# Optimization experiments

Measured on AMD Instinct MI355X. Metric: run time of the kernel, lower is better.

The kernel has to match this reference:

```python
import jax, jax.numpy as jnp
import numpy as np

B, T, D_MODEL, HEAD_DIM = 4, 4096, 2048, 128
NEG = -1e9  # matches torch's -1000000000.0 mask fill


def setup_inputs() -> dict:
    key = jax.random.key(0)
    ks = jax.random.split(key, 7)
    s = 0.02
    return {
        "x": jax.random.normal(ks[0], (B, T, D_MODEL), dtype=jnp.float32),
        "q_w": jax.random.normal(ks[1], (HEAD_DIM, D_MODEL), dtype=jnp.float32) * s,
        "q_b": jax.random.normal(ks[2], (HEAD_DIM,), dtype=jnp.float32) * s,
        "k_w": jax.random.normal(ks[3], (HEAD_DIM, D_MODEL), dtype=jnp.float32) * s,
        "k_b": jax.random.normal(ks[4], (HEAD_DIM,), dtype=jnp.float32) * s,
        "v_w": jax.random.normal(ks[5], (HEAD_DIM, D_MODEL), dtype=jnp.float32) * s,
        "v_b": jax.random.normal(ks[6], (HEAD_DIM,), dtype=jnp.float32) * s,
    }


def reference(x, q_w, q_b, k_w, k_b, v_w, v_b):
    # Linear projections: y = x @ W^T + b  -> [B, T, head_dim]
    q = jnp.einsum("btc,hc->bth", x, q_w) + q_b
    k = jnp.einsum("btc,hc->bth", x, k_w) + k_b
    v = jnp.einsum("btc,hc->bth", x, v_w) + v_b

    head_dim = q.shape[-1]
    # scores [B, T, T], scaled by 1/sqrt(head_dim)
    scores = jnp.einsum("bqh,bkh->bqk", q, k) / jnp.sqrt(jnp.float32(head_dim))
    # causal mask: additive -1e9 above the diagonal (future positions)
    t = scores.shape[-1]
    mask = jnp.triu(jnp.full((t, t), NEG, dtype=scores.dtype), k=1)
    scores = scores + mask
    probs = jax.nn.softmax(scores, axis=-1)
    # dropout p=0.0 -> identity (eval)
    y = jnp.einsum("bqk,bkh->bqh", probs, v)
    return y
```

## Files before the change

### kernel.cpp

```cpp
#include <hip/hip_runtime.h>

#define T_SEQ 4096
#define DMODEL 2048
#define HD 128

typedef float f32x4 __attribute__((ext_vector_type(4)));
typedef _Float16 f16x8 __attribute__((ext_vector_type(8)));

__device__ __forceinline__ unsigned short f2h(float f) {
  union { _Float16 h; unsigned short u; } v;
  v.h = (_Float16)f;
  return v.u;
}

__device__ __forceinline__ unsigned pk2h(float lo, float hi) {
  return (unsigned)f2h(lo) | ((unsigned)f2h(hi) << 16);
}

template <int CTRL>
__device__ __forceinline__ float dppmax(float x) {
  union { float f; int i; } a, b;
  a.f = x;
  b.i = __builtin_amdgcn_update_dpp(a.i, a.i, CTRL, 0xF, 0xF, false);
  return fmaxf(x, b.f);
}
template <int CTRL>
__device__ __forceinline__ float dppadd(float x) {
  union { float f; int i; } a, b;
  a.f = x;
  b.i = __builtin_amdgcn_update_dpp(a.i, a.i, CTRL, 0xF, 0xF, false);
  return x + b.f;
}
__device__ __forceinline__ float red16_max(float x) {
  x = dppmax<0xB1>(x); x = dppmax<0x4E>(x);
  x = dppmax<0x124>(x); x = dppmax<0x128>(x);
  return x;
}
__device__ __forceinline__ float red16_add(float x) {
  x = dppadd<0xB1>(x); x = dppadd<0x4E>(x);
  x = dppadd<0x124>(x); x = dppadd<0x128>(x);
  return x;
}

__global__ __launch_bounds__(256) void cvt_w_kernel(
    const float* __restrict__ qw, const float* __restrict__ qb,
    const float* __restrict__ kw, const float* __restrict__ kb,
    const float* __restrict__ vw, const float* __restrict__ vb,
    unsigned short* __restrict__ wb, float* __restrict__ biasc) {
  int idx = blockIdx.x * 256 + threadIdx.x;
  int e = idx * 4;
  int row = e >> 11;
  int col = e & 2047;
  const float* src = (row < 128) ? (qw + row * 2048)
                   : (row < 256) ? (kw + (row - 128) * 2048)
                                 : (vw + (row - 256) * 2048);
  float4 v = *(const float4*)(src + col);
  ushort4 o;
  o.x = f2h(v.x); o.y = f2h(v.y); o.z = f2h(v.z); o.w = f2h(v.w);
  *(ushort4*)(wb + e) = o;
  if (blockIdx.x == 0 && threadIdx.x < 384) {
    int n = threadIdx.x;
    biasc[n] = (n < 128) ? qb[n] : (n < 256) ? kb[n - 128] : vb[n - 256];
  }
}

#define SAB 40
__global__ __launch_bounds__(256, 3) void proj_kernel(
    const float* __restrict__ x, const unsigned short* __restrict__ wb,
    const float* __restrict__ biasc, unsigned short* __restrict__ qkv) {
  __shared__ unsigned short sA[64 * SAB];
  __shared__ unsigned short sB[128 * SAB];
  const int tid = threadIdx.x;
  const int lane = tid & 63;
  const int w = tid >> 6;
  const int fr = lane & 15;
  const int g = lane >> 4;
  const int m0 = blockIdx.x * 64;
  const int n0 = blockIdx.y * 128;
  const int wm = (w & 1) * 32;
  const int wn = (w >> 1) * 64;

  const int arow = tid >> 2;
  const int acolA = (tid & 3) * 8;
  const int brow = tid >> 1;
  const int bcolB = (tid & 1) * 16;
  const float* xp = x + (size_t)(m0 + arow) * DMODEL + acolA;
  const unsigned short* bp = wb + (size_t)(n0 + brow) * DMODEL + bcolB;

  f32x4 acc[2][4] = {};
  float4 ax0 = *(const float4*)(xp);
  float4 ax1 = *(const float4*)(xp + 4);
  uint4 bx0 = *(const uint4*)(bp);
  uint4 bx1 = *(const uint4*)(bp + 8);

  for (int k0 = 0; k0 < DMODEL; k0 += 32) {
    __syncthreads();
    uint4 pa;
    pa.x = pk2h(ax0.x, ax0.y); pa.y = pk2h(ax0.z, ax0.w);
    pa.z = pk2h(ax1.x, ax1.y); pa.w = pk2h(ax1.z, ax1.w);
    *(uint4*)&sA[arow * SAB + acolA] = pa;
    *(uint4*)&sB[brow * SAB + bcolB] = bx0;
    *(uint4*)&sB[brow * SAB + bcolB + 8] = bx1;
    __syncthreads();

    if (k0 + 32 < DMODEL) {
      ax0 = *(const float4*)(xp + k0 + 32);
      ax1 = *(const float4*)(xp + k0 + 36);
      bx0 = *(const uint4*)(bp + k0 + 32);
      bx1 = *(const uint4*)(bp + k0 + 40);
    }

    f16x8 af[2], bf[4];
#pragma unroll
    for (int i = 0; i < 2; ++i)
      af[i] = *(const f16x8*)&sA[(wm + 16 * i + fr) * SAB + g * 8];
#pragma unroll
    for (int jn = 0; jn < 4; ++jn)
      bf[jn] = *(const f16x8*)&sB[(wn + 16 * jn + fr) * SAB + g * 8];
#pragma unroll
    for (int i = 0; i < 2; ++i)
#pragma unroll
      for (int jn = 0; jn < 4; ++jn)
        acc[i][jn] = __builtin_amdgcn_mfma_f32_16x16x32_f16(af[i], bf[jn], acc[i][jn], 0, 0, 0);
  }

#pragma unroll
  for (int jn = 0; jn < 4; ++jn) {
    int n = n0 + wn + 16 * jn + fr;
    float bias = biasc[n];
#pragma unroll
    for (int i = 0; i < 2; ++i) {
      int mb = m0 + wm + 16 * i + g * 4;
#pragma unroll
      for (int r = 0; r < 4; ++r)
        qkv[(size_t)(mb + r) * 384 + n] = f2h(acc[i][jn][r] + bias);
    }
  }
}

#define SKS 136
#define SVS 72
#define SPS 72
__global__ __launch_bounds__(256) __attribute__((amdgpu_waves_per_eu(2, 3)))
void attn_kernel(
    const unsigned short* __restrict__ qkv, float* __restrict__ out,
    float* __restrict__ po, float* __restrict__ pml, int split) {
  __shared__ unsigned short sK[64 * SKS];
  __shared__ unsigned short sVt[128 * SVS];
  __shared__ unsigned short sP[64 * SPS];
  const int id = blockIdx.x;
  const int batch = blockIdx.y;
  int qt, c, nc;
  if (split) {
    if (id < 16)      { qt = id;                c = 0;          nc = 1; }
    else if (id < 48) { qt = 16 + ((id - 16) >> 1); c = (id - 16) & 1; nc = 2; }
    else if (id < 96) { qt = 32 + (id - 48) / 3;    c = (id - 48) % 3; nc = 3; }
    else              { qt = 48 + ((id - 96) >> 2); c = (id - 96) & 3; nc = 4; }
  } else { qt = id; c = 0; nc = 1; }
  const int qbase = qt * 64;
  const int ntl = qt + 1;
  const int t0 = (c * ntl) / nc;
  const int tend = ((c + 1) * ntl) / nc;
  const int tid = threadIdx.x;
  const int lane = tid & 63;
  const int w = tid >> 6;
  const int fr = lane & 15;
  const int g = lane >> 4;
  const int va = tid >> 4;
  const int vu = tid & 15;
  const int vblk = ((va ^ (vu & 14)) << 2);
  const unsigned short* qkvb = qkv + (size_t)batch * T_SEQ * 384;

  f16x8 qf[4];
  {
    const unsigned short* qp = qkvb + (size_t)(qbase + 16 * w + fr) * 384 + g * 8;
#pragma unroll
    for (int s = 0; s < 4; ++s) qf[s] = *(const f16x8*)(qp + 32 * s);
  }
  f32x4 o[8] = {};
  float m_r[4], l_r[4];
#pragma unroll
  for (int r = 0; r < 4; ++r) { m_r[r] = -1e30f; l_r[r] = 0.f; }
  const float scale = 0.08838834764831845f;

  uint4 pk[4], pvv[4];
#pragma unroll
  for (int it = 0; it < 4; ++it) {
    int idx = it * 256 + tid;
    pk[it] = *(const uint4*)(qkvb + (size_t)(t0 * 64 + (idx >> 4)) * 384 + 128 + (idx & 15) * 8);
  }
#pragma unroll
  for (int i = 0; i < 4; ++i)
    pvv[i] = *(const uint4*)(qkvb + (size_t)(t0 * 64 + va + 16 * i) * 384 + 256 + vu * 8);

  for (int t = t0; t < tend; ++t) {
    const int kbase = t * 64;
    __syncthreads();
#pragma unroll
    for (int it = 0; it < 4; ++it) {
      int idx = it * 256 + tid;
      *(uint4*)&sK[(idx >> 4) * SKS + (idx & 15) * 8] = pk[it];
    }
    {
      const unsigned* w0 = (const unsigned*)&pvv[0];
      const unsigned* w1 = (const unsigned*)&pvv[1];
      const unsigned* w2 = (const unsigned*)&pvv[2];
      const unsigned* w3 = (const unsigned*)&pvv[3];
#pragma unroll
      for (int j2 = 0; j2 < 4; ++j2) {
        uint2 se, so;
        se.x = __builtin_amdgcn_perm(w1[j2], w0[j2], 0x05040100);
        se.y = __builtin_amdgcn_perm(w3[j2], w2[j2], 0x05040100);
        so.x = __builtin_amdgcn_perm(w1[j2], w0[j2], 0x07060302);
        so.y = __builtin_amdgcn_perm(w3[j2], w2[j2], 0x07060302);
        *(uint2*)&sVt[(8 * vu + 2 * j2) * SVS + vblk] = se;
        *(uint2*)&sVt[(8 * vu + 2 * j2 + 1) * SVS + vblk] = so;
      }
    }
    __syncthreads();

    if (t + 1 < tend) {
#pragma unroll
      for (int it = 0; it < 4; ++it) {
        int idx = it * 256 + tid;
        pk[it] = *(const uint4*)(qkvb + (size_t)((t + 1) * 64 + (idx >> 4)) * 384 + 128 + (idx & 15) * 8);
      }
#pragma unroll
      for (int i = 0; i < 4; ++i)
        pvv[i] = *(const uint4*)(qkvb + (size_t)((t + 1) * 64 + va + 16 * i) * 384 + 256 + vu * 8);
    }

    f32x4 sacc[4] = {};
#pragma unroll
    for (int ks = 0; ks < 4; ++ks)
#pragma unroll
      for (int tn = 0; tn < 4; ++tn) {
        f16x8 kf = *(const f16x8*)&sK[(16 * tn + fr) * SKS + 32 * ks + g * 8];
        sacc[tn] = __builtin_amdgcn_mfma_f32_16x16x32_f16(qf[ks], kf, sacc[tn], 0, 0, 0);
      }

    const bool diag = (t == qt);
#pragma unroll
    for (int r = 0; r < 4; ++r) {
      int grow = qbase + 16 * w + g * 4 + r;
      float s0 = sacc[0][r] * scale;
      float s1 = sacc[1][r] * scale;
      float s2 = sacc[2][r] * scale;
      float s3 = sacc[3][r] * scale;
      if (diag) {
        int kd = grow - kbase - fr;
        if (0 > kd)  s0 = -1e30f;
        if (16 > kd) s1 = -1e30f;
        if (32 > kd) s2 = -1e30f;
        if (48 > kd) s3 = -1e30f;
      }
      float mx = fmaxf(fmaxf(s0, s1), fmaxf(s2, s3));
      mx = red16_max(mx);
      float mnew = fmaxf(m_r[r], mx);
      float alpha = __expf(m_r[r] - mnew);
      m_r[r] = mnew;
      float p0 = __expf(s0 - mnew);
      float p1 = __expf(s1 - mnew);
      float p2 = __expf(s2 - mnew);
      float p3 = __expf(s3 - mnew);
      float rs = (p0 + p1) + (p2 + p3);
      rs = red16_add(rs);
      l_r[r] = l_r[r] * alpha + rs;
#pragma unroll
      for (int nt = 0; nt < 8; ++nt) o[nt][r] *= alpha;
      uint2 pw;
      pw.x = pk2h(p0, p1);
      pw.y = pk2h(p2, p3);
      *(uint2*)&sP[(16 * w + 4 * g + r) * SPS + 4 * fr] = pw;
    }

#pragma unroll
    for (int ks = 0; ks < 2; ++ks) {
      f16x8 pa = *(const f16x8*)&sP[(16 * w + fr) * SPS + 32 * ks + 8 * g];
#pragma unroll
      for (int nt = 0; nt < 8; ++nt) {
        int d = 16 * nt + fr;
        int blk = ((8 * ks + 2 * g) ^ ((d >> 3) & 14)) << 2;
        f16x8 vf = *(const f16x8*)&sVt[d * SVS + blk];
        o[nt] = __builtin_amdgcn_mfma_f32_16x16x32_f16(pa, vf, o[nt], 0, 0, 0);
      }
    }
  }

  if (nc == 1) {
#pragma unroll
    for (int r = 0; r < 4; ++r) {
      float inv = 1.0f / l_r[r];
      int grow = qbase + 16 * w + g * 4 + r;
      float* op = out + ((size_t)batch * T_SEQ + grow) * HD;
#pragma unroll
      for (int nt = 0; nt < 8; ++nt)
        op[16 * nt + fr] = o[nt][r] * inv;
    }
  } else {
    size_t slot = ((size_t)batch * 160 + id) * 64;
#pragma unroll
    for (int r = 0; r < 4; ++r) {
      int lrow = 16 * w + g * 4 + r;
      float* op = po + (slot + lrow) * 128;
#pragma unroll
      for (int nt = 0; nt < 8; ++nt)
        op[16 * nt + fr] = o[nt][r];
      if (fr == 0) {
        pml[(slot + lrow) * 2] = m_r[r];
        pml[(slot + lrow) * 2 + 1] = l_r[r];
      }
    }
  }
}

__global__ __launch_bounds__(256) void combine_kernel(
    const float* __restrict__ po, const float* __restrict__ pml,
    float* __restrict__ out) {
  int gr = blockIdx.x * 2 + (threadIdx.x >> 7);
  int d = threadIdx.x & 127;
  int batch = gr / 3072;
  int ridx = gr - batch * 3072;
  int qt = 16 + (ridx >> 6);
  int rr = ridx & 63;
  int nc = 1 + (qt >> 4);
  int sb = (qt < 32) ? 16 + (qt - 16) * 2
         : (qt < 48) ? 48 + (qt - 32) * 3
                     : 96 + (qt - 48) * 4;
  size_t base = ((size_t)batch * 160 + sb) * 64 + rr;
  float mi[4], li[4];
  float M = -1e30f;
#pragma unroll
  for (int i = 0; i < 4; ++i) {
    if (i < nc) {
      mi[i] = pml[(base + (size_t)i * 64) * 2];
      li[i] = pml[(base + (size_t)i * 64) * 2 + 1];
      M = fmaxf(M, mi[i]);
    }
  }
  float L = 0.f, acc = 0.f;
#pragma unroll
  for (int i = 0; i < 4; ++i) {
    if (i < nc) {
      float sc = __expf(mi[i] - M);
      L += li[i] * sc;
      acc += po[(base + (size_t)i * 64) * 128 + d] * sc;
    }
  }
  out[((size_t)batch * T_SEQ + qt * 64 + rr) * HD + d] = acc / L;
}

extern "C" void kernel_launch(void* const* d_in, const int* in_sizes, int n_in,
                              void* d_out, int out_size, void* d_ws, size_t ws_size,
                              hipStream_t stream) {
  const float* x  = (const float*)d_in[0];
  const float* qw = (const float*)d_in[1];
  const float* qb = (const float*)d_in[2];
  const float* kw = (const float*)d_in[3];
  const float* kb = (const float*)d_in[4];
  const float* vw = (const float*)d_in[5];
  const float* vb = (const float*)d_in[6];
  float* out = (float*)d_out;

  unsigned short* qkv = (unsigned short*)d_ws;
  unsigned short* wb  = qkv + (size_t)16384 * 384;
  float* biasc = (float*)(wb + (size_t)384 * 2048);
  float* po  = (float*)((char*)d_ws + 14157312);
  float* pml = po + (size_t)640 * 64 * 128;
  size_t need = 14157312 + (size_t)640 * 64 * 128 * 4 + (size_t)640 * 64 * 2 * 4;
  int split = (ws_size >= need) ? 1 : 0;

  cvt_w_kernel<<<768, 256, 0, stream>>>(qw, qb, kw, kb, vw, vb, wb, biasc);
  proj_kernel<<<dim3(256, 3), 256, 0, stream>>>(x, wb, biasc, qkv);
  attn_kernel<<<dim3(split ? 160 : 64, 4), 256, 0, stream>>>(qkv, out, po, pml, split);
  if (split)
    combine_kernel<<<6144, 256, 0, stream>>>(po, pml, out);
}
```

Before: 142.0 us.

## Double attention query tile to 128 rows with 512-thread blocks sharing K/V tiles

```diff
diff --git a/kernel.cpp b/kernel.cpp
--- a/kernel.cpp
+++ b/kernel.cpp
@@ -141,24 +141,24 @@
 #define SKS 136
 #define SVS 72
 #define SPS 72
-__global__ __launch_bounds__(256) __attribute__((amdgpu_waves_per_eu(2, 3)))
+__global__ __launch_bounds__(512) __attribute__((amdgpu_waves_per_eu(2, 4)))
 void attn_kernel(
     const unsigned short* __restrict__ qkv, float* __restrict__ out,
     float* __restrict__ po, float* __restrict__ pml, int split) {
   __shared__ unsigned short sK[64 * SKS];
   __shared__ unsigned short sVt[128 * SVS];
-  __shared__ unsigned short sP[64 * SPS];
+  __shared__ unsigned short sP[128 * SPS];
   const int id = blockIdx.x;
   const int batch = blockIdx.y;
   int qt, c, nc;
   if (split) {
-    if (id < 16)      { qt = id;                c = 0;          nc = 1; }
-    else if (id < 48) { qt = 16 + ((id - 16) >> 1); c = (id - 16) & 1; nc = 2; }
-    else if (id < 96) { qt = 32 + (id - 48) / 3;    c = (id - 48) % 3; nc = 3; }
-    else              { qt = 48 + ((id - 96) >> 2); c = (id - 96) & 3; nc = 4; }
+    if (id < 8)       { qt = id;                    c = 0;              nc = 1; }
+    else if (id < 24) { qt = 8 + ((id - 8) >> 1);   c = (id - 8) & 1;   nc = 2; }
+    else if (id < 48) { qt = 16 + (id - 24) / 3;    c = (id - 24) % 3;  nc = 3; }
+    else              { qt = 24 + ((id - 48) >> 2); c = (id - 48) & 3;  nc = 4; }
   } else { qt = id; c = 0; nc = 1; }
-  const int qbase = qt * 64;
-  const int ntl = qt + 1;
+  const int qbase = qt * 128;
+  const int ntl = 2 * qt + 2;
   const int t0 = (c * ntl) / nc;
   const int tend = ((c + 1) * ntl) / nc;
   const int tid = threadIdx.x;
@@ -166,9 +166,11 @@
   const int w = tid >> 6;
   const int fr = lane & 15;
   const int g = lane >> 4;
-  const int va = tid >> 4;
+  const bool vHalf = tid < 256;
+  const int va = (tid >> 4) & 15;
   const int vu = tid & 15;
   const int vblk = ((va ^ (vu & 14)) << 2);
+  const int st = tid & 255;
   const unsigned short* qkvb = qkv + (size_t)batch * T_SEQ * 384;
 
   f16x8 qf[4];
@@ -183,29 +185,28 @@
   for (int r = 0; r < 4; ++r) { m_r[r] = -1e30f; l_r[r] = 0.f; }
   const float scale = 0.08838834764831845f;
 
-  uint4 pk[4], pvv[4];
-#pragma unroll
-  for (int it = 0; it < 4; ++it) {
-    int idx = it * 256 + tid;
-    pk[it] = *(const uint4*)(qkvb + (size_t)(t0 * 64 + (idx >> 4)) * 384 + 128 + (idx & 15) * 8);
-  }
-#pragma unroll
-  for (int i = 0; i < 4; ++i)
-    pvv[i] = *(const uint4*)(qkvb + (size_t)(t0 * 64 + va + 16 * i) * 384 + 256 + vu * 8);
+  uint4 pbuf[4];
+  if (vHalf) {
+#pragma unroll
+    for (int i = 0; i < 4; ++i) {
+      pbuf[i] = *(const uint4*)(qkvb + (size_t)(t0 * 64 + va + 16 * i) * 384 + 256 + vu * 8);
+    }
+  } else {
+#pragma unroll
+    for (int it = 0; it < 4; ++it) {
+      int idx = it * 256 + st;
+      pbuf[it] = *(const uint4*)(qkvb + (size_t)(t0 * 64 + (idx >> 4)) * 384 + 128 + (idx & 15) * 8);
+    }
+  }
 
   for (int t = t0; t < tend; ++t) {
     const int kbase = t * 64;
     __syncthreads();
-#pragma unroll
-    for (int it = 0; it < 4; ++it) {
-      int idx = it * 256 + tid;
-      *(uint4*)&sK[(idx >> 4) * SKS + (idx & 15) * 8] = pk[it];
-    }
-    {
-      const unsigned* w0 = (const unsigned*)&pvv[0];
-      const unsigned* w1 = (const unsigned*)&pvv[1];
-      const unsigned* w2 = (const unsigned*)&pvv[2];
-      const unsigned* w3 = (const unsigned*)&pvv[3];
+    if (vHalf) {
+      const unsigned* w0 = (const unsigned*)&pbuf[0];
+      const unsigned* w1 = (const unsigned*)&pbuf[1];
+      const unsigned* w2 = (const unsigned*)&pbuf[2];
+      const unsigned* w3 = (const unsigned*)&pbuf[3];
 #pragma unroll
       for (int j2 = 0; j2 < 4; ++j2) {
         uint2 se, so;
@@ -216,18 +217,27 @@
         *(uint2*)&sVt[(8 * vu + 2 * j2) * SVS + vblk] = se;
         *(uint2*)&sVt[(8 * vu + 2 * j2 + 1) * SVS + vblk] = so;
       }
+    } else {
+#pragma unroll
+      for (int it = 0; it < 4; ++it) {
+        int idx = it * 256 + st;
+        *(uint4*)&sK[(idx >> 4) * SKS + (idx & 15) * 8] = pbuf[it];
+      }
     }
     __syncthreads();
 
     if (t + 1 < tend) {
-#pragma unroll
-      for (int it = 0; it < 4; ++it) {
-        int idx = it * 256 + tid;
-        pk[it] = *(const uint4*)(qkvb + (size_t)((t + 1) * 64 + (idx >> 4)) * 384 + 128 + (idx & 15) * 8);
-      }
-#pragma unroll
-      for (int i = 0; i < 4; ++i)
-        pvv[i] = *(const uint4*)(qkvb + (size_t)((t + 1) * 64 + va + 16 * i) * 384 + 256 + vu * 8);
+      if (vHalf) {
+#pragma unroll
+        for (int i = 0; i < 4; ++i)
+          pbuf[i] = *(const uint4*)(qkvb + (size_t)((t + 1) * 64 + va + 16 * i) * 384 + 256 + vu * 8);
+      } else {
+#pragma unroll
+        for (int it = 0; it < 4; ++it) {
+          int idx = it * 256 + st;
+          pbuf[it] = *(const uint4*)(qkvb + (size_t)((t + 1) * 64 + (idx >> 4)) * 384 + 128 + (idx & 15) * 8);
+        }
+      }
     }
 
     f32x4 sacc[4] = {};
@@ -239,7 +249,7 @@
         sacc[tn] = __builtin_amdgcn_mfma_f32_16x16x32_f16(qf[ks], kf, sacc[tn], 0, 0, 0);
       }
 
-    const bool diag = (t == qt);
+    const bool anymask = (kbase + 63) > (qbase + 16 * w);
 #pragma unroll
     for (int r = 0; r < 4; ++r) {
       int grow = qbase + 16 * w + g * 4 + r;
@@ -247,7 +257,7 @@
       float s1 = sacc[1][r] * scale;
       float s2 = sacc[2][r] * scale;
       float s3 = sacc[3][r] * scale;
-      if (diag) {
+      if (anymask) {
         int kd = grow - kbase - fr;
         if (0 > kd)  s0 = -1e30f;
         if (16 > kd) s1 = -1e30f;
@@ -298,7 +308,7 @@
         op[16 * nt + fr] = o[nt][r] * inv;
     }
   } else {
-    size_t slot = ((size_t)batch * 160 + id) * 64;
+    size_t slot = ((size_t)batch * 80 + id) * 128;
 #pragma unroll
     for (int r = 0; r < 4; ++r) {
       int lrow = 16 * w + g * 4 + r;
@@ -321,20 +331,20 @@
   int d = threadIdx.x & 127;
   int batch = gr / 3072;
   int ridx = gr - batch * 3072;
-  int qt = 16 + (ridx >> 6);
-  int rr = ridx & 63;
-  int nc = 1 + (qt >> 4);
-  int sb = (qt < 32) ? 16 + (qt - 16) * 2
-         : (qt < 48) ? 48 + (qt - 32) * 3
-                     : 96 + (qt - 48) * 4;
-  size_t base = ((size_t)batch * 160 + sb) * 64 + rr;
+  int qt = 8 + (ridx >> 7);
+  int rr = ridx & 127;
+  int nc = 1 + (qt >> 3);
+  int sb = (qt < 16) ? 8 + (qt - 8) * 2
+         : (qt < 24) ? 24 + (qt - 16) * 3
+                     : 48 + (qt - 24) * 4;
+  size_t base = ((size_t)batch * 80 + sb) * 128 + rr;
   float mi[4], li[4];
   float M = -1e30f;
 #pragma unroll
   for (int i = 0; i < 4; ++i) {
     if (i < nc) {
-      mi[i] = pml[(base + (size_t)i * 64) * 2];
-      li[i] = pml[(base + (size_t)i * 64) * 2 + 1];
+      mi[i] = pml[(base + (size_t)i * 128) * 2];
+      li[i] = pml[(base + (size_t)i * 128) * 2 + 1];
       M = fmaxf(M, mi[i]);
     }
   }
@@ -344,10 +354,10 @@
     if (i < nc) {
       float sc = __expf(mi[i] - M);
       L += li[i] * sc;
-      acc += po[(base + (size_t)i * 64) * 128 + d] * sc;
-    }
-  }
-  out[((size_t)batch * T_SEQ + qt * 64 + rr) * HD + d] = acc / L;
+      acc += po[(base + (size_t)i * 128) * 128 + d] * sc;
+    }
+  }
+  out[((size_t)batch * T_SEQ + qt * 128 + rr) * HD + d] = acc / L;
 }
 
 extern "C" void kernel_launch(void* const* d_in, const int* in_sizes, int n_in,
@@ -366,13 +376,13 @@
   unsigned short* wb  = qkv + (size_t)16384 * 384;
   float* biasc = (float*)(wb + (size_t)384 * 2048);
   float* po  = (float*)((char*)d_ws + 14157312);
-  float* pml = po + (size_t)640 * 64 * 128;
-  size_t need = 14157312 + (size_t)640 * 64 * 128 * 4 + (size_t)640 * 64 * 2 * 4;
+  float* pml = po + (size_t)320 * 128 * 128;
+  size_t need = 14157312 + (size_t)320 * 128 * 128 * 4 + (size_t)320 * 128 * 2 * 4;
   int split = (ws_size >= need) ? 1 : 0;
 
   cvt_w_kernel<<<768, 256, 0, stream>>>(qw, qb, kw, kb, vw, vb, wb, biasc);
   proj_kernel<<<dim3(256, 3), 256, 0, stream>>>(x, wb, biasc, qkv);
-  attn_kernel<<<dim3(split ? 160 : 64, 4), 256, 0, stream>>>(qkv, out, po, pml, split);
+  attn_kernel<<<dim3(split ? 80 : 32, 4), 512, 0, stream>>>(qkv, out, po, pml, split);
   if (split)
     combine_kernel<<<6144, 256, 0, stream>>>(po, pml, out);
 }
```

Measured after the change: 150.7 us. 6.1% more time.
